# Performance work log

Hardware: AMD Instinct MI355X
Metric: run time of the kernel (lower is better)

Reference implementation:

```python
import jax, jax.numpy as jnp
import numpy as np

D_MODEL = 1024
NHEAD = 16
D_HEAD = D_MODEL // NHEAD
DIM_FF = 4096
EPS = 1e-5

def layer_norm(x, scale, bias):
    mu = jnp.mean(x, axis=-1, keepdims=True)
    var = jnp.mean(jnp.square(x - mu), axis=-1, keepdims=True)
    return (x - mu) * jax.lax.rsqrt(var + EPS) * scale + bias

def setup_inputs() -> dict:
    key = jax.random.key(0)
    ks = jax.random.split(key, 8)
    B, T, D = 4, 2048, D_MODEL
    s = 1.0 / np.sqrt(D)
    sf = 1.0 / np.sqrt(DIM_FF)
    return {
        "x": jax.random.normal(ks[0], (B, T, D), dtype=jnp.float32),
        "ln1_scale": jnp.ones((D,), jnp.float32),
        "ln1_bias": jnp.zeros((D,), jnp.float32),
        "qkv_w": jax.random.normal(ks[1], (3 * D, D), jnp.float32) * s,  # torch Linear weight [out,in]
        "out_w": jax.random.normal(ks[2], (D, D), jnp.float32) * s,
        "ln2_scale": jnp.ones((D,), jnp.float32),
        "ln2_bias": jnp.zeros((D,), jnp.float32),
        "fc1_w": jax.random.normal(ks[3], (DIM_FF, D), jnp.float32) * s,
        "fc1_b": jnp.zeros((DIM_FF,), jnp.float32),
        "fc2_w": jax.random.normal(ks[4], (D, DIM_FF), jnp.float32) * sf,
        "fc2_b": jnp.zeros((D,), jnp.float32),
    }

def reference(x, ln1_scale, ln1_bias, qkv_w, out_w, ln2_scale, ln2_bias, fc1_w, fc1_b, fc2_w, fc2_b):
    B, T, D = x.shape
    # --- attention sublayer (pre-LN) ---
    h = layer_norm(x, ln1_scale, ln1_bias)
    qkv = jnp.einsum('btd,ed->bte', h, qkv_w)  # [B,T,3D]
    q, k, v = jnp.split(qkv, 3, axis=-1)
    def heads(t):
        return t.reshape(B, T, NHEAD, D_HEAD).transpose(0, 2, 1, 3)  # [B,H,T,dh]
    q, k, v = heads(q), heads(k), heads(v)
    scores = jnp.einsum('bhqd,bhkd->bhqk', q, k) / np.sqrt(D_HEAD)
    attn = jax.nn.softmax(scores, axis=-1)
    o = jnp.einsum('bhqk,bhkd->bhqd', attn, v)
    o = o.transpose(0, 2, 1, 3).reshape(B, T, D)
    h = jnp.einsum('btd,ed->bte', o, out_w)
    x = x + h
    # --- FFN sublayer (pre-LN) ---
    h = layer_norm(x, ln2_scale, ln2_bias)
    h = jnp.einsum('btd,fd->btf', h, fc1_w) + fc1_b
    h = jax.nn.gelu(h, approximate=False)
    h = jnp.einsum('btf,df->btd', h, fc2_w) + fc2_b
    return x + h
```

## Files before the change

kernel.cpp:

```cpp
#include <hip/hip_runtime.h>
#include <hip/hip_bf16.h>
#include <math.h>

typedef unsigned short u16;
typedef unsigned int u32;
typedef short s8v __attribute__((ext_vector_type(8)));
typedef float f4v __attribute__((ext_vector_type(4)));
typedef float f16v __attribute__((ext_vector_type(16)));
typedef u32 u4v __attribute__((ext_vector_type(4)));
typedef u32 u2v __attribute__((ext_vector_type(2)));

#define D_MODEL 1024
#define DIMFF   4096
#define SEQ     2048
#define TOKENS  8192

#define QSCALE 0.18033688011112042f

static __device__ __forceinline__ u16 f2bf(float f) {
    unsigned int u = __builtin_bit_cast(unsigned int, f);
    unsigned int lsb = (u >> 16) & 1u;
    u += 0x7fffu + lsb;
    return (u16)(u >> 16);
}

static __device__ __forceinline__ float gelu_fast(float z) {
    float z2 = z * z;
    float p  = fmaf(z2, -0.1029472255f, -2.3021867892f);
    float e  = __builtin_amdgcn_exp2f(z * p);
    return z * __builtin_amdgcn_rcpf(1.0f + e);
}

static __device__ __forceinline__ void gl2lds16(const u16* g, u16* l) {
    __builtin_amdgcn_global_load_lds(
        (__attribute__((address_space(1))) void*)(void*)g,
        (__attribute__((address_space(3))) void*)l, 16, 0, 0);
}

static __device__ __forceinline__ void bar() {
    __builtin_amdgcn_sched_barrier(0);
    asm volatile("" ::: "memory");
    __builtin_amdgcn_s_barrier();
    asm volatile("" ::: "memory");
    __builtin_amdgcn_sched_barrier(0);
}

template<int N> static __device__ __forceinline__ void vwait() {
    if constexpr (N == 4)       asm volatile("s_waitcnt vmcnt(4)" ::: "memory");
    else if constexpr (N == 8)  asm volatile("s_waitcnt vmcnt(8)" ::: "memory");
    else if constexpr (N == 12) asm volatile("s_waitcnt vmcnt(12)" ::: "memory");
    else                        asm volatile("s_waitcnt vmcnt(0)" ::: "memory");
}

#define N4_QKV  786432
#define N4_WO   262144
#define N4_FC   1048576
__global__ __launch_bounds__(256) void cvt_all_kernel(const float* __restrict__ s0,
                                                      const float* __restrict__ s1,
                                                      const float* __restrict__ s2,
                                                      const float* __restrict__ s3,
                                                      u16* __restrict__ dst) {
    int i = blockIdx.x * 256 + threadIdx.x;
    const float* src; int j;
    if (i < N4_QKV)                    { src = s0; j = i; }
    else if (i < N4_QKV + N4_WO)       { src = s1; j = i - N4_QKV; }
    else if (i < N4_QKV + N4_WO + N4_FC) { src = s2; j = i - N4_QKV - N4_WO; }
    else                               { src = s3; j = i - N4_QKV - N4_WO - N4_FC; }
    float4 v = ((const float4*)src)[j];
    ushort4 o;
    o.x = f2bf(v.x); o.y = f2bf(v.y); o.z = f2bf(v.z); o.w = f2bf(v.w);
    ((ushort4*)dst)[i] = o;
}

__global__ __launch_bounds__(256) void ln_kernel(const float* __restrict__ x,
                                                 const float* __restrict__ scale,
                                                 const float* __restrict__ bias,
                                                 u16* __restrict__ out) {
    int row = blockIdx.x;
    int t = threadIdx.x;
    const float* xr = x + (size_t)row * D_MODEL;
    float4 v = ((const float4*)xr)[t];
    float s  = v.x + v.y + v.z + v.w;
    float ss = v.x*v.x + v.y*v.y + v.z*v.z + v.w*v.w;
    #pragma unroll
    for (int off = 1; off < 64; off <<= 1) {
        s  += __shfl_xor(s, off);
        ss += __shfl_xor(ss, off);
    }
    __shared__ float red[8];
    int wave = t >> 6, lane = t & 63;
    if (lane == 0) { red[wave] = s; red[4 + wave] = ss; }
    __syncthreads();
    float S  = red[0] + red[1] + red[2] + red[3];
    float SS = red[4] + red[5] + red[6] + red[7];
    float mu  = S * (1.0f / D_MODEL);
    float var = SS * (1.0f / D_MODEL) - mu * mu;
    float r = rsqrtf(var + 1e-5f);
    float4 sc = ((const float4*)scale)[t];
    float4 bi = ((const float4*)bias)[t];
    ushort4 o;
    o.x = f2bf((v.x - mu) * r * sc.x + bi.x);
    o.y = f2bf((v.y - mu) * r * sc.y + bi.y);
    o.z = f2bf((v.z - mu) * r * sc.z + bi.z);
    o.w = f2bf((v.w - mu) * r * sc.w + bi.w);
    ((ushort4*)(out + (size_t)row * D_MODEL))[t] = o;
}

template<int MODE, int DEPTH>
__global__ __launch_bounds__(256, 2) void gemm_kernel(
        const u16* __restrict__ A, const u16* __restrict__ W,
        const float* __restrict__ bias, const float* __restrict__ res,
        void* __restrict__ outp, void* __restrict__ out2, int M, int N, int K) {
    constexpr int BM = 128, BN_ = 128, BK = 32;
    constexpr int RA = 2;
    constexpr int RB = 2;
    constexpr int S = DEPTH - 1;
    constexpr int VST = (S - 2) * (RA + RB);
    constexpr int ASZ = BM * BK, BSZ = BN_ * BK;
    __shared__ __attribute__((aligned(16))) u16 As[DEPTH * ASZ];
    __shared__ __attribute__((aligned(16))) u16 Bs[DEPTH * BSZ];

    int t = threadIdx.x;
    int lane = t & 63, w = t >> 6;
    int lc = lane & 15, lr = lane >> 4;
    int xcd = blockIdx.x & 7, li = blockIdx.x >> 3;
    int bm = xcd * 8 + (li & 7), bn = li >> 3;
    int m0 = bm * BM, n0 = bn * BN_;
    int wm = (w & 1) * 64;
    int wn = (w >> 1) * 64;
    int cxor = (lr ^ ((lc >> 1) & 3)) * 8;

    const u16* Abase = A + (size_t)m0 * K;
    const u16* Bbase = W + (size_t)n0 * K;

    size_t aoff[RA]; int aldo[RA];
    #pragma unroll
    for (int n = 0; n < RA; ++n) {
        int q = (n * 4 + w) * 64 + lane;
        int row = q >> 2;
        aoff[n] = (size_t)row * K + (((q & 3) ^ ((row >> 1) & 3)) * 8);
        aldo[n] = (n * 4 + w) * 512;
    }
    size_t boff[RB]; int bldo[RB];
    #pragma unroll
    for (int n = 0; n < RB; ++n) {
        int q = (n * 4 + w) * 64 + lane;
        int row = q >> 2;
        boff[n] = (size_t)row * K + (((q & 3) ^ ((row >> 1) & 3)) * 8);
        bldo[n] = (n * 4 + w) * 512;
    }

    const int NT = K / BK;
    for (int u = 0; u < S; ++u) {
        size_t kk = (size_t)u * BK;
        #pragma unroll
        for (int n = 0; n < RA; ++n) gl2lds16(Abase + aoff[n] + kk, &As[u * ASZ + aldo[n]]);
        #pragma unroll
        for (int n = 0; n < RB; ++n) gl2lds16(Bbase + boff[n] + kk, &Bs[u * BSZ + bldo[n]]);
    }
    vwait<VST>();
    bar();

    f4v acc[4][4] = {};
    s8v afA[4], bA_[4], afB[4], bB_[4];
    #pragma unroll
    for (int i = 0; i < 4; ++i)
        afA[i] = *(const s8v*)&As[(wm + i * 16 + lc) * BK + cxor];
    #pragma unroll
    for (int j = 0; j < 4; ++j)
        bA_[j] = *(const s8v*)&Bs[(wn + j * 16 + lc) * BK + cxor];
    int rs = 1, ss = S;

#define GSTEP(T, AFL, BL, AFC, BC)                                            \
    {                                                                         \
        const u16* Ab = &As[rs * ASZ];                                        \
        const u16* Bb = &Bs[rs * BSZ];                                        \
        _Pragma("unroll")                                                     \
        for (int i = 0; i < 4; ++i)                                           \
            AFL[i] = *(const s8v*)&Ab[(wm + i * 16 + lc) * BK + cxor];        \
        _Pragma("unroll")                                                     \
        for (int j = 0; j < 4; ++j)                                           \
            BL[j] = *(const s8v*)&Bb[(wn + j * 16 + lc) * BK + cxor];         \
        int kts = (T) + S; if (kts > NT - 1) kts = NT - 1;                    \
        size_t kk = (size_t)kts * BK;                                         \
        _Pragma("unroll")                                                     \
        for (int n = 0; n < RA; ++n)                                          \
            gl2lds16(Abase + aoff[n] + kk, &As[ss * ASZ + aldo[n]]);          \
        _Pragma("unroll")                                                     \
        for (int n = 0; n < RB; ++n)                                          \
            gl2lds16(Bbase + boff[n] + kk, &Bs[ss * BSZ + bldo[n]]);          \
        __builtin_amdgcn_s_setprio(1);                                        \
        _Pragma("unroll")                                                     \
        for (int i = 0; i < 4; ++i) {                                         \
            _Pragma("unroll")                                                 \
            for (int j = 0; j < 4; ++j) {                                     \
                if constexpr (MODE == 4)                                      \
                    acc[i][j] = __builtin_amdgcn_mfma_f32_16x16x32_bf16(AFC[i], BC[j], acc[i][j], 0, 0, 0); \
                else                                                          \
                    acc[i][j] = __builtin_amdgcn_mfma_f32_16x16x32_bf16(BC[j], AFC[i], acc[i][j], 0, 0, 0); \
            }                                                                 \
        }                                                                     \
        __builtin_amdgcn_s_setprio(0);                                        \
        vwait<VST>();                                                         \
        bar();                                                                \
        rs = (rs + 1 == DEPTH) ? 0 : rs + 1;                                  \
        ss = (ss + 1 == DEPTH) ? 0 : ss + 1;                                  \
    }

    for (int kt = 0; kt < NT; kt += 2) {
        GSTEP(kt,     afB, bB_, afA, bA_)
        GSTEP(kt + 1, afA, bA_, afB, bB_)
    }
#undef GSTEP

    if constexpr (MODE == 4) {
        #pragma unroll
        for (int i = 0; i < 4; ++i) {
            #pragma unroll
            for (int j = 0; j < 4; ++j) {
                int col = n0 + wn + j * 16 + lc;
                int colbase = n0 + wn + j * 16;
                if (colbase < 2048) {
                    float sc = (colbase < 1024) ? QSCALE : 1.0f;
                    #pragma unroll
                    for (int r = 0; r < 4; ++r) {
                        int row = m0 + wm + i * 16 + lr * 4 + r;
                        ((u16*)outp)[(size_t)row * 2048 + col] = f2bf(acc[i][j][r] * sc);
                    }
                } else {
                    int dlin = col - 2048;
                    int h = dlin >> 6, dd = dlin & 63;
                    int trow = m0 + wm + i * 16 + lr * 4;
                    int bb = trow >> 11, tt = trow & 2047;
                    int bh = bb * 16 + h;
                    ushort4 vv;
                    vv.x = f2bf(acc[i][j][0]); vv.y = f2bf(acc[i][j][1]);
                    vv.z = f2bf(acc[i][j][2]); vv.w = f2bf(acc[i][j][3]);
                    *(ushort4*)&((u16*)out2)[((size_t)bh * 64 + dd) * SEQ + tt] = vv;
                }
            }
        }
    } else {
        #pragma unroll
        for (int j = 0; j < 4; ++j) {
            int colb = n0 + wn + j * 16 + lr * 4;
            float4 b4;
            if constexpr (MODE != 1) b4 = *(const float4*)&bias[colb];
            #pragma unroll
            for (int i = 0; i < 4; ++i) {
                int row = m0 + wm + i * 16 + lc;
                size_t idx = (size_t)row * N + colb;
                f4v a = acc[i][j];
                if constexpr (MODE == 2) {
                    ushort4 o;
                    o.x = f2bf(gelu_fast(a[0] + b4.x));
                    o.y = f2bf(gelu_fast(a[1] + b4.y));
                    o.z = f2bf(gelu_fast(a[2] + b4.z));
                    o.w = f2bf(gelu_fast(a[3] + b4.w));
                    *(ushort4*)&((u16*)outp)[idx] = o;
                } else {
                    float4 rr = *(const float4*)&res[idx];
                    float4 o;
                    if constexpr (MODE == 3) {
                        o.x = rr.x + a[0] + b4.x; o.y = rr.y + a[1] + b4.y;
                        o.z = rr.z + a[2] + b4.z; o.w = rr.w + a[3] + b4.w;
                    } else {
                        o.x = rr.x + a[0]; o.y = rr.y + a[1];
                        o.z = rr.z + a[2]; o.w = rr.w + a[3];
                    }
                    *(float4*)&((float*)outp)[idx] = o;
                }
            }
        }
    }
}

__global__ __launch_bounds__(256) void attn_kernel(const u16* __restrict__ qk,
                                                   const u16* __restrict__ vt,
                                                   u16* __restrict__ out) {
    __shared__ __attribute__((aligned(16))) u16 Ks[64 * 64];
    __shared__ __attribute__((aligned(16))) u16 Vts[64 * 64];
    __shared__ float l_s[128];
    int t = threadIdx.x, lane = t & 63, w = t >> 6;
    int l31 = lane & 31, hi = lane >> 5;
    int blk = blockIdx.x;
    int bh = blk & 63, qt = blk >> 6;
    int b = bh >> 4, h = bh & 15;
    size_t tok0 = (size_t)b * SEQ;
    int q0 = qt * 128;

    s8v bq[4];
    {
        const u16* qp = qk + (tok0 + q0 + w * 32 + l31) * 2048 + h * 64 + hi * 8;
        #pragma unroll
        for (int dch = 0; dch < 4; ++dch) bq[dch] = *(const s8v*)(qp + dch * 16);
    }
    f16v o[2] = {};
    float lp = 0.f;

    int srow[2], scg[2];
    #pragma unroll
    for (int n = 0; n < 2; ++n) {
        int chunk = (w * 2 + n) * 64 + lane;
        srow[n] = chunk >> 3;
        scg[n]  = ((chunk & 7) ^ (srow[n] & 7)) * 8;
    }
    const u16* vbase = vt + (size_t)bh * 64 * SEQ;

    for (int kt = 0; kt < SEQ / 64; ++kt) {
        #pragma unroll
        for (int n = 0; n < 2; ++n) {
            gl2lds16(&qk[(tok0 + kt * 64 + srow[n]) * 2048 + 1024 + h * 64 + scg[n]],
                     &Ks[(w * 2 + n) * 512]);
            gl2lds16(&vbase[(size_t)srow[n] * SEQ + kt * 64 + scg[n]],
                     &Vts[(w * 2 + n) * 512]);
        }
        __syncthreads();

        f16v s_[2] = {};
        #pragma unroll
        for (int kb = 0; kb < 2; ++kb)
            #pragma unroll
            for (int dch = 0; dch < 4; ++dch) {
                s8v ak = *(const s8v*)&Ks[(kb * 32 + l31) * 64 + ((dch * 2 + hi) ^ (l31 & 7)) * 8];
                s_[kb] = __builtin_amdgcn_mfma_f32_32x32x16_bf16(ak, bq[dch], s_[kb], 0, 0, 0);
            }

        u2v pk[2][4];
        #pragma unroll
        for (int kb = 0; kb < 2; ++kb)
            #pragma unroll
            for (int g = 0; g < 4; ++g) {
                u32 ib[4];
                #pragma unroll
                for (int rr = 0; rr < 4; ++rr) {
                    ib[rr] = (u32)fmaf(s_[kb][g * 4 + rr], 8388608.0f, 1064992506.0f);
                    lp += __builtin_bit_cast(float, ib[rr]);
                }
                pk[kb][g][0] = __builtin_amdgcn_perm(ib[1], ib[0], 0x07060302);
                pk[kb][g][1] = __builtin_amdgcn_perm(ib[3], ib[2], 0x07060302);
            }

        #pragma unroll
        for (int ch = 0; ch < 4; ++ch) {
            int kb = ch >> 1, a2 = (ch & 1) * 2;
            u2v sx = __builtin_amdgcn_permlane32_swap(pk[kb][a2][0], pk[kb][a2 + 1][0], false, false);
            u2v sy = __builtin_amdgcn_permlane32_swap(pk[kb][a2][1], pk[kb][a2 + 1][1], false, false);
            u4v tmp; tmp.x = sx[0]; tmp.y = sy[0]; tmp.z = sx[1]; tmp.w = sy[1];
            s8v ap = __builtin_bit_cast(s8v, tmp);
            #pragma unroll
            for (int dblk = 0; dblk < 2; ++dblk) {
                s8v bv = *(const s8v*)&Vts[(dblk * 32 + l31) * 64 + ((ch * 2 + hi) ^ (l31 & 7)) * 8];
                o[dblk] = __builtin_amdgcn_mfma_f32_32x32x16_bf16(ap, bv, o[dblk], 0, 0, 0);
            }
        }
        __syncthreads();
    }

    lp += __shfl_xor(lp, 32);
    l_s[w * 32 + l31] = 1.0f / lp;
    #pragma unroll
    for (int r = 0; r < 16; ++r) {
        int qrl = (r & 3) + 8 * (r >> 2) + 4 * hi;
        float linv = l_s[w * 32 + qrl];
        size_t row = tok0 + q0 + w * 32 + qrl;
        #pragma unroll
        for (int dblk = 0; dblk < 2; ++dblk)
            out[row * 1024 + h * 64 + dblk * 32 + l31] = f2bf(o[dblk][r] * linv);
    }
}

extern "C" void kernel_launch(void* const* d_in, const int* in_sizes, int n_in,
                              void* d_out, int out_size, void* d_ws, size_t ws_size,
                              hipStream_t stream) {
    const float* x      = (const float*)d_in[0];
    const float* ln1_s  = (const float*)d_in[1];
    const float* ln1_b  = (const float*)d_in[2];
    const float* qkv_w  = (const float*)d_in[3];
    const float* out_w  = (const float*)d_in[4];
    const float* ln2_s  = (const float*)d_in[5];
    const float* ln2_b  = (const float*)d_in[6];
    const float* fc1_w  = (const float*)d_in[7];
    const float* fc1_b  = (const float*)d_in[8];
    const float* fc2_w  = (const float*)d_in[9];
    const float* fc2_b  = (const float*)d_in[10];
    float* out = (float*)d_out;

    char* ws = (char*)d_ws;
    size_t off = 0;
    auto alloc = [&](size_t bytes) -> void* {
        void* p = ws + off;
        off += (bytes + 255) & ~(size_t)255;
        return p;
    };
    u16* wq  = (u16*)alloc((size_t)3072 * 1024 * 2);
    u16* wo  = (u16*)alloc((size_t)1024 * 1024 * 2);
    u16* w1  = (u16*)alloc((size_t)4096 * 1024 * 2);
    u16* w2  = (u16*)alloc((size_t)1024 * 4096 * 2);
    u16* h1  = (u16*)alloc((size_t)TOKENS * 1024 * 2);
    u16* qk  = (u16*)alloc((size_t)TOKENS * 2048 * 2);
    float* x2 = (float*)alloc((size_t)TOKENS * 1024 * 4);
    u16* g   = (u16*)alloc((size_t)TOKENS * 4096 * 2);
    u16* attn_out = h1;
    u16* h2       = qk;
    u16* vt       = (u16*)x2;
    (void)wo; (void)w1; (void)w2;

    cvt_all_kernel<<<(N4_QKV + N4_WO + 2 * N4_FC) / 256, 256, 0, stream>>>(
        qkv_w, out_w, fc1_w, fc2_w, wq);

    ln_kernel<<<TOKENS, 256, 0, stream>>>(x, ln1_s, ln1_b, h1);
    gemm_kernel<4, 4><<<(TOKENS / 128) * (3072 / 128), 256, 0, stream>>>(
        h1, wq, nullptr, nullptr, qk, vt, TOKENS, 3072, 1024);
    attn_kernel<<<64 * 16, 256, 0, stream>>>(qk, vt, attn_out);
    gemm_kernel<1, 4><<<(TOKENS / 128) * (1024 / 128), 256, 0, stream>>>(
        attn_out, wo, nullptr, x, x2, nullptr, TOKENS, 1024, 1024);
    ln_kernel<<<TOKENS, 256, 0, stream>>>(x2, ln2_s, ln2_b, h2);
    gemm_kernel<2, 4><<<(TOKENS / 128) * (DIMFF / 128), 256, 0, stream>>>(
        h2, w1, fc1_b, nullptr, g, nullptr, TOKENS, DIMFF, 1024);
    gemm_kernel<3, 4><<<(TOKENS / 128) * (1024 / 128), 256, 0, stream>>>(
        g, w2, fc2_b, x2, out, nullptr, TOKENS, 1024, DIMFF);
}
```

Baseline: 508.4 us.

## Load GEMM A operand directly to registers, stage only B in LDS

The GEMM now loads A-operand fragments directly from global memory into registers, prefetched one k-tile ahead. Only the weight (B) tile is staged through LDS, using a 3-buffer ring with BK=64 and an XOR swizzle. This removes the LDS traffic and space for A and halves the number of barriers per K. In exchange, A is reloaded redundantly across waves, depends on L2, and global latency is exposed on the A path.

```diff
diff --git a/kernel.cpp b/kernel.cpp
--- a/kernel.cpp
+++ b/kernel.cpp
@@ -46,9 +46,8 @@
 }
 
 template<int N> static __device__ __forceinline__ void vwait() {
-    if constexpr (N == 4)       asm volatile("s_waitcnt vmcnt(4)" ::: "memory");
+    if constexpr (N == 12)      asm volatile("s_waitcnt vmcnt(12)" ::: "memory");
     else if constexpr (N == 8)  asm volatile("s_waitcnt vmcnt(8)" ::: "memory");
-    else if constexpr (N == 12) asm volatile("s_waitcnt vmcnt(12)" ::: "memory");
     else                        asm volatile("s_waitcnt vmcnt(0)" ::: "memory");
 }
 
@@ -106,110 +105,97 @@
     ((ushort4*)(out + (size_t)row * D_MODEL))[t] = o;
 }
 
-template<int MODE, int DEPTH>
+template<int MODE>
 __global__ __launch_bounds__(256, 2) void gemm_kernel(
         const u16* __restrict__ A, const u16* __restrict__ W,
         const float* __restrict__ bias, const float* __restrict__ res,
         void* __restrict__ outp, void* __restrict__ out2, int M, int N, int K) {
-    constexpr int BM = 128, BN_ = 128, BK = 32;
-    constexpr int RA = 2;
-    constexpr int RB = 2;
-    constexpr int S = DEPTH - 1;
-    constexpr int VST = (S - 2) * (RA + RB);
-    constexpr int ASZ = BM * BK, BSZ = BN_ * BK;
-    __shared__ __attribute__((aligned(16))) u16 As[DEPTH * ASZ];
-    __shared__ __attribute__((aligned(16))) u16 Bs[DEPTH * BSZ];
+    constexpr int BN_ = 128, BK = 64;
+    constexpr int BSZ = BN_ * BK;
+    __shared__ __attribute__((aligned(16))) u16 Bs[3][BSZ];
 
     int t = threadIdx.x;
     int lane = t & 63, w = t >> 6;
     int lc = lane & 15, lr = lane >> 4;
     int xcd = blockIdx.x & 7, li = blockIdx.x >> 3;
     int bm = xcd * 8 + (li & 7), bn = li >> 3;
-    int m0 = bm * BM, n0 = bn * BN_;
-    int wm = (w & 1) * 64;
-    int wn = (w >> 1) * 64;
-    int cxor = (lr ^ ((lc >> 1) & 3)) * 8;
-
-    const u16* Abase = A + (size_t)m0 * K;
+    int m0 = bm * 128, n0 = bn * BN_;
+    int wm = (w & 1) * 64, wn = (w >> 1) * 64;
+
+    const u16* Alane = A + (size_t)(m0 + wm + lc) * K + lr * 8;
     const u16* Bbase = W + (size_t)n0 * K;
 
-    size_t aoff[RA]; int aldo[RA];
-    #pragma unroll
-    for (int n = 0; n < RA; ++n) {
-        int q = (n * 4 + w) * 64 + lane;
-        int row = q >> 2;
-        aoff[n] = (size_t)row * K + (((q & 3) ^ ((row >> 1) & 3)) * 8);
-        aldo[n] = (n * 4 + w) * 512;
-    }
-    size_t boff[RB]; int bldo[RB];
-    #pragma unroll
-    for (int n = 0; n < RB; ++n) {
-        int q = (n * 4 + w) * 64 + lane;
-        int row = q >> 2;
-        boff[n] = (size_t)row * K + (((q & 3) ^ ((row >> 1) & 3)) * 8);
-        bldo[n] = (n * 4 + w) * 512;
-    }
-
-    const int NT = K / BK;
-    for (int u = 0; u < S; ++u) {
-        size_t kk = (size_t)u * BK;
-        #pragma unroll
-        for (int n = 0; n < RA; ++n) gl2lds16(Abase + aoff[n] + kk, &As[u * ASZ + aldo[n]]);
-        #pragma unroll
-        for (int n = 0; n < RB; ++n) gl2lds16(Bbase + boff[n] + kk, &Bs[u * BSZ + bldo[n]]);
-    }
-    vwait<VST>();
+    int boff[4], bldo[4];
+    #pragma unroll
+    for (int n = 0; n < 4; ++n) {
+        int opid = n * 4 + w;
+        int row = opid * 8 + (lane >> 3);
+        boff[n] = row * K + ((lane & 7) ^ (row & 7)) * 8;
+        bldo[n] = opid * 512;
+    }
+
+    const int NK = K / BK;
+    const int NKm1 = NK - 1;
+    #pragma unroll
+    for (int n = 0; n < 4; ++n) gl2lds16(Bbase + boff[n], &Bs[0][bldo[n]]);
+    #pragma unroll
+    for (int n = 0; n < 4; ++n) gl2lds16(Bbase + boff[n] + 64, &Bs[1][bldo[n]]);
+    f4v acc[4][4] = {};
+    s8v afA[4][2], afB[4][2], bf[4][2];
+    #pragma unroll
+    for (int i = 0; i < 4; ++i)
+        #pragma unroll
+        for (int ks = 0; ks < 2; ++ks)
+            afA[i][ks] = *(const s8v*)&Alane[(size_t)i * 16 * K + ks * 32];
+    vwait<0>();
     bar();
 
-    f4v acc[4][4] = {};
-    s8v afA[4], bA_[4], afB[4], bB_[4];
-    #pragma unroll
-    for (int i = 0; i < 4; ++i)
-        afA[i] = *(const s8v*)&As[(wm + i * 16 + lc) * BK + cxor];
-    #pragma unroll
-    for (int j = 0; j < 4; ++j)
-        bA_[j] = *(const s8v*)&Bs[(wn + j * 16 + lc) * BK + cxor];
-    int rs = 1, ss = S;
-
-#define GSTEP(T, AFL, BL, AFC, BC)                                            \
+    const u16* Br = Bs[0];
+    u16* Bn = (u16*)Bs[1];
+    u16* Bss = (u16*)Bs[2];
+
+#define GSTEP(T, AFC, AFN)                                                    \
     {                                                                         \
-        const u16* Ab = &As[rs * ASZ];                                        \
-        const u16* Bb = &Bs[rs * BSZ];                                        \
+        int tn = (T) + 1; if (tn > NKm1) tn = NKm1;                           \
+        int ts = (T) + 2; if (ts > NKm1) ts = NKm1;                           \
         _Pragma("unroll")                                                     \
         for (int i = 0; i < 4; ++i)                                           \
-            AFL[i] = *(const s8v*)&Ab[(wm + i * 16 + lc) * BK + cxor];        \
+            _Pragma("unroll")                                                 \
+            for (int ks = 0; ks < 2; ++ks)                                    \
+                AFN[i][ks] = *(const s8v*)&Alane[(size_t)i * 16 * K + ks * 32 + (size_t)tn * 64]; \
         _Pragma("unroll")                                                     \
-        for (int j = 0; j < 4; ++j)                                           \
-            BL[j] = *(const s8v*)&Bb[(wn + j * 16 + lc) * BK + cxor];         \
-        int kts = (T) + S; if (kts > NT - 1) kts = NT - 1;                    \
-        size_t kk = (size_t)kts * BK;                                         \
+        for (int n = 0; n < 4; ++n)                                           \
+            gl2lds16(Bbase + boff[n] + (size_t)ts * 64, Bss + bldo[n]);       \
         _Pragma("unroll")                                                     \
-        for (int n = 0; n < RA; ++n)                                          \
-            gl2lds16(Abase + aoff[n] + kk, &As[ss * ASZ + aldo[n]]);          \
-        _Pragma("unroll")                                                     \
-        for (int n = 0; n < RB; ++n)                                          \
-            gl2lds16(Bbase + boff[n] + kk, &Bs[ss * BSZ + bldo[n]]);          \
+        for (int j = 0; j < 4; ++j) {                                         \
+            int brow = wn + j * 16 + lc;                                      \
+            _Pragma("unroll")                                                 \
+            for (int ks = 0; ks < 2; ++ks)                                    \
+                bf[j][ks] = *(const s8v*)&Br[brow * 64 + ((ks * 4 + lr) ^ (brow & 7)) * 8]; \
+        }                                                                     \
+        asm volatile("s_waitcnt lgkmcnt(0)" ::: "memory");                    \
+        vwait<12>();                                                          \
+        __builtin_amdgcn_sched_barrier(0);                                    \
         __builtin_amdgcn_s_setprio(1);                                        \
         _Pragma("unroll")                                                     \
-        for (int i = 0; i < 4; ++i) {                                         \
+        for (int ks = 0; ks < 2; ++ks)                                        \
             _Pragma("unroll")                                                 \
-            for (int j = 0; j < 4; ++j) {                                     \
-                if constexpr (MODE == 4)                                      \
-                    acc[i][j] = __builtin_amdgcn_mfma_f32_16x16x32_bf16(AFC[i], BC[j], acc[i][j], 0, 0, 0); \
-                else                                                          \
-                    acc[i][j] = __builtin_amdgcn_mfma_f32_16x16x32_bf16(BC[j], AFC[i], acc[i][j], 0, 0, 0); \
-            }                                                                 \
-        }                                                                     \
+            for (int i = 0; i < 4; ++i)                                       \
+                _Pragma("unroll")                                             \
+                for (int j = 0; j < 4; ++j) {                                 \
+                    if constexpr (MODE == 4)                                  \
+                        acc[i][j] = __builtin_amdgcn_mfma_f32_16x16x32_bf16(AFC[i][ks], bf[j][ks], acc[i][j], 0, 0, 0); \
+                    else                                                      \
+                        acc[i][j] = __builtin_amdgcn_mfma_f32_16x16x32_bf16(bf[j][ks], AFC[i][ks], acc[i][j], 0, 0, 0); \
+                }                                                             \
         __builtin_amdgcn_s_setprio(0);                                        \
-        vwait<VST>();                                                         \
         bar();                                                                \
-        rs = (rs + 1 == DEPTH) ? 0 : rs + 1;                                  \
-        ss = (ss + 1 == DEPTH) ? 0 : ss + 1;                                  \
-    }
-
-    for (int kt = 0; kt < NT; kt += 2) {
-        GSTEP(kt,     afB, bB_, afA, bA_)
-        GSTEP(kt + 1, afA, bA_, afB, bB_)
+        u16* tmpB = (u16*)Br; Br = Bn; Bn = Bss; Bss = tmpB;                  \
+    }
+
+    for (int kt = 0; kt < NK; kt += 2) {
+        GSTEP(kt,     afA, afB)
+        GSTEP(kt + 1, afB, afA)
     }
 #undef GSTEP
 
@@ -410,14 +396,14 @@
         qkv_w, out_w, fc1_w, fc2_w, wq);
 
     ln_kernel<<<TOKENS, 256, 0, stream>>>(x, ln1_s, ln1_b, h1);
-    gemm_kernel<4, 4><<<(TOKENS / 128) * (3072 / 128), 256, 0, stream>>>(
+    gemm_kernel<4><<<(TOKENS / 128) * (3072 / 128), 256, 0, stream>>>(
         h1, wq, nullptr, nullptr, qk, vt, TOKENS, 3072, 1024);
     attn_kernel<<<64 * 16, 256, 0, stream>>>(qk, vt, attn_out);
-    gemm_kernel<1, 4><<<(TOKENS / 128) * (1024 / 128), 256, 0, stream>>>(
+    gemm_kernel<1><<<(TOKENS / 128) * (1024 / 128), 256, 0, stream>>>(
         attn_out, wo, nullptr, x, x2, nullptr, TOKENS, 1024, 1024);
     ln_kernel<<<TOKENS, 256, 0, stream>>>(x2, ln2_s, ln2_b, h2);
-    gemm_kernel<2, 4><<<(TOKENS / 128) * (DIMFF / 128), 256, 0, stream>>>(
+    gemm_kernel<2><<<(TOKENS / 128) * (DIMFF / 128), 256, 0, stream>>>(
         h2, w1, fc1_b, nullptr, g, nullptr, TOKENS, DIMFF, 1024);
-    gemm_kernel<3, 4><<<(TOKENS / 128) * (1024 / 128), 256, 0, stream>>>(
+    gemm_kernel<3><<<(TOKENS / 128) * (1024 / 128), 256, 0, stream>>>(
         g, w2, fc2_b, x2, out, nullptr, TOKENS, 1024, DIMFF);
 }
```

New measurement: 704.5 us. 1.39x slower.
